# Kernel optimization log

Measured on AMD Instinct MI355X. Metric: run time of the kernel, lower is better.

Reference implementation:

```python
import jax, jax.numpy as jnp
import numpy as np

NT, NJ = 100000, 300000
FT = FJ = 32
H, OUT = 64, 16
E_TJ = E_JT = 1000000
E_JJ = 2000000
# NormalParamExtractor default: biased_softplus(1.0) -> softplus(x + inv_softplus(1.0))
SP_BIAS = float(np.log(np.expm1(1.0)))


def setup_inputs() -> dict:
    key = jax.random.key(0)
    ks = jax.random.split(key, 64)
    ki = iter(range(64))
    def nrm(shape, fan_in):
        return jax.random.normal(ks[next(ki)], shape, jnp.float32) / np.sqrt(fan_in)
    d = {}
    d['x_torso'] = jax.random.normal(ks[next(ki)], (NT, FT), jnp.float32)
    d['x_joint'] = jax.random.normal(ks[next(ki)], (NJ, FJ), jnp.float32)
    def edges(e, n_src, n_dst):
        src = jax.random.randint(ks[next(ki)], (e,), 0, n_src, jnp.int32)
        dst = jax.random.randint(ks[next(ki)], (e,), 0, n_dst, jnp.int32)
        return jnp.stack([src, dst])
    d['ei_tj'] = edges(E_TJ, NT, NJ)
    d['ei_jt'] = edges(E_JT, NJ, NT)
    d['ei_jj'] = edges(E_JJ, NJ, NJ)
    d['w0_t'] = nrm((FT, H), FT); d['b0_t'] = jnp.zeros((H,), jnp.float32)
    d['w0_j'] = nrm((FJ, H), FJ); d['b0_j'] = jnp.zeros((H,), jnp.float32)
    for layer in ('c1', 'c2'):
        for et in ('tj', 'jt', 'jj'):
            d[f'{layer}_{et}_rel_w'] = nrm((H, H), H)
            d[f'{layer}_{et}_rel_b'] = jnp.zeros((H,), jnp.float32)
            d[f'{layer}_{et}_root_w'] = nrm((H, H), H)
    d['w3_t'] = nrm((H, OUT), H); d['b3_t'] = jnp.zeros((OUT,), jnp.float32)
    d['w3_j'] = nrm((H, OUT), H); d['b3_j'] = jnp.zeros((OUT,), jnp.float32)
    return d


def _graph_conv(x_src, x_dst, ei, rel_w, rel_b, root_w, n_dst):
    # PyG GraphConv: lin_rel(sum_{j in N(i)} x_j) + lin_root(x_i)
    msg = jax.ops.segment_sum(x_src[ei[0]], ei[1], num_segments=n_dst)
    return msg @ rel_w + rel_b + x_dst @ root_w


def reference(x_torso, x_joint, ei_tj, ei_jt, ei_jj,
              w0_t, b0_t, w0_j, b0_j,
              c1_tj_rel_w, c1_tj_rel_b, c1_tj_root_w,
              c1_jt_rel_w, c1_jt_rel_b, c1_jt_root_w,
              c1_jj_rel_w, c1_jj_rel_b, c1_jj_root_w,
              c2_tj_rel_w, c2_tj_rel_b, c2_tj_root_w,
              c2_jt_rel_w, c2_jt_rel_b, c2_jt_root_w,
              c2_jj_rel_w, c2_jj_rel_b, c2_jj_root_w,
              w3_t, b3_t, w3_j, b3_j):
    # per-node-type input Linear
    h_t = x_torso @ w0_t + b0_t  # [NT, 64]
    h_j = x_joint @ w0_j + b0_j  # [NJ, 64]
    # hetero GraphConv layer 1 (to_hetero sums per-edge-type outputs on dst)
    t1 = _graph_conv(h_j, h_t, ei_jt, c1_jt_rel_w, c1_jt_rel_b, c1_jt_root_w, NT)
    j1 = (_graph_conv(h_t, h_j, ei_tj, c1_tj_rel_w, c1_tj_rel_b, c1_tj_root_w, NJ)
          + _graph_conv(h_j, h_j, ei_jj, c1_jj_rel_w, c1_jj_rel_b, c1_jj_root_w, NJ))
    h_t, h_j = jnp.tanh(t1), jnp.tanh(j1)
    # layer 2
    t2 = _graph_conv(h_j, h_t, ei_jt, c2_jt_rel_w, c2_jt_rel_b, c2_jt_root_w, NT)
    j2 = (_graph_conv(h_t, h_j, ei_tj, c2_tj_rel_w, c2_tj_rel_b, c2_tj_root_w, NJ)
          + _graph_conv(h_j, h_j, ei_jj, c2_jj_rel_w, c2_jj_rel_b, c2_jj_root_w, NJ))
    h_t, h_j = jnp.tanh(t2), jnp.tanh(j2)
    # output Linear + tanh per node type
    o_t = jnp.tanh(h_t @ w3_t + b3_t)  # [NT, 16]
    o_j = jnp.tanh(h_j @ w3_j + b3_j)  # [NJ, 16]
    # NormalParamExtractor: chunk last dim, biased softplus on scale
    loc_t, s_t = jnp.split(o_t, 2, axis=-1)
    loc_j, s_j = jnp.split(o_j, 2, axis=-1)
    scale_t = jax.nn.softplus(s_t + SP_BIAS)
    scale_j = jax.nn.softplus(s_j + SP_BIAS)
    return (loc_t, scale_t, loc_j, scale_j)
```

## Files before the change

### kernel.cpp

```cpp
#include <hip/hip_runtime.h>
#include <math.h>

constexpr int NT = 100000;
constexpr int NJ = 300000;
constexpr int E_TJ = 1000000, E_JT = 1000000, E_JJ = 2000000;
constexpr float SP_BIAS = 0.5413248546129181f;

__global__ void k_zero(int* __restrict__ p, int n) {
    int i = blockIdx.x * 256 + threadIdx.x;
    if (i < n) p[i] = 0;
}

__global__ void k_prep(const float* __restrict__ wa, const float* __restrict__ wb,
                       const float* __restrict__ ba, const float* __restrict__ bb,
                       float* __restrict__ wcomb, float* __restrict__ bcomb) {
    int i = blockIdx.x * 256 + threadIdx.x;
    if (i < 4096) wcomb[i] = wa[i] + wb[i];
    else if (i < 4160) bcomb[i - 4096] = ba[i - 4096] + bb[i - 4096];
}

__global__ void k_count(const int* __restrict__ dst, int E, int* __restrict__ deg) {
    int e = blockIdx.x * blockDim.x + threadIdx.x;
    if (e < E) atomicAdd(&deg[dst[e]], 1);
}

__global__ __launch_bounds__(1024) void k_bsum(const int* __restrict__ deg, int n,
                                               int* __restrict__ bsum) {
    __shared__ int s[1024];
    int i = blockIdx.x * 1024 + threadIdx.x;
    s[threadIdx.x] = (i < n) ? deg[i] : 0;
    __syncthreads();
    for (int d = 512; d > 0; d >>= 1) {
        if (threadIdx.x < d) s[threadIdx.x] += s[threadIdx.x + d];
        __syncthreads();
    }
    if (threadIdx.x == 0) bsum[blockIdx.x] = s[0];
}

__global__ __launch_bounds__(1024) void k_scan_bsum(int* bsum, int nb) {
    __shared__ int s[1024];
    int t = threadIdx.x;
    int v = (t < nb) ? bsum[t] : 0;
    s[t] = v;
    __syncthreads();
    for (int d = 1; d < 1024; d <<= 1) {
        int x = (t >= d) ? s[t - d] : 0;
        __syncthreads();
        s[t] += x;
        __syncthreads();
    }
    if (t < nb) bsum[t] = s[t] - v;
}

__global__ __launch_bounds__(1024) void k_scan_final(const int* __restrict__ deg, int n,
                                                     const int* __restrict__ bsum,
                                                     int* __restrict__ off,
                                                     int* __restrict__ cur) {
    __shared__ int s[1024];
    int t = threadIdx.x;
    int i = blockIdx.x * 1024 + t;
    int v = (i < n) ? deg[i] : 0;
    s[t] = v;
    __syncthreads();
    for (int d = 1; d < 1024; d <<= 1) {
        int x = (t >= d) ? s[t - d] : 0;
        __syncthreads();
        s[t] += x;
        __syncthreads();
    }
    int incl = s[t];
    int base = bsum[blockIdx.x];
    if (i < n) {
        int excl = base + incl - v;
        off[i] = excl;
        cur[i] = excl;
        if (i == n - 1) off[n] = base + incl;
    }
}

__global__ void k_fill(const int* __restrict__ src, const int* __restrict__ dst, int E,
                       int* __restrict__ cur, int* __restrict__ out_src, int src_ofs) {
    int e = blockIdx.x * blockDim.x + threadIdx.x;
    if (e < E) {
        int p = atomicAdd(&cur[dst[e]], 1);
        out_src[p] = (src[e] + src_ofs) * 64;
    }
}

__global__ __launch_bounds__(256) void k_in_linear(const float* __restrict__ x,
        const float* __restrict__ w, const float* __restrict__ b,
        float* __restrict__ h, int n) {
    __shared__ float ws_[32 * 64];
    __shared__ __align__(16) float xs_[512];
    for (int i = threadIdx.x; i < 32 * 64; i += 256) ws_[i] = w[i];
    __syncthreads();
    const int wslot = (threadIdx.x >> 6) & 3;
    const int lane = threadIdx.x & 63;
    const int lo = lane & 31;
    float* xsw = &xs_[wslot * 128];
    int wave = (blockIdx.x * 256 + threadIdx.x) >> 6;
    int nq = (n + 3) >> 2;
    int nwaves = gridDim.x * 4;
    float bv = b[lane];
    for (int q = wave; q < nq; q += nwaves) {
        int i0 = q * 4;
        int i1 = i0 + 1 < n ? i0 + 1 : n - 1;
        int i2 = i0 + 2 < n ? i0 + 2 : n - 1;
        int i3 = i0 + 3 < n ? i0 + 3 : n - 1;
        xsw[lane]      = (lane < 32) ? x[(size_t)i0 * 32 + lo] : x[(size_t)i1 * 32 + lo];
        xsw[64 + lane] = (lane < 32) ? x[(size_t)i2 * 32 + lo] : x[(size_t)i3 * 32 + lo];
        float r0 = bv, r1 = bv, r2 = bv, r3 = bv;
        const float4* xq = (const float4*)xsw;
        #pragma unroll
        for (int c = 0; c < 8; ++c) {
            float4 x0 = xq[c], x1 = xq[8 + c], x2 = xq[16 + c], x3 = xq[24 + c];
            float wA = ws_[(4 * c + 0) * 64 + lane];
            float wB = ws_[(4 * c + 1) * 64 + lane];
            float wC = ws_[(4 * c + 2) * 64 + lane];
            float wD = ws_[(4 * c + 3) * 64 + lane];
            r0 += x0.x * wA + x0.y * wB + x0.z * wC + x0.w * wD;
            r1 += x1.x * wA + x1.y * wB + x1.z * wC + x1.w * wD;
            r2 += x2.x * wA + x2.y * wB + x2.z * wC + x2.w * wD;
            r3 += x3.x * wA + x3.y * wB + x3.z * wC + x3.w * wD;
        }
        h[(size_t)i0 * 64 + lane] = r0;
        if (i0 + 1 < n) h[(size_t)i1 * 64 + lane] = r1;
        if (i0 + 2 < n) h[(size_t)i2 * 64 + lane] = r2;
        if (i0 + 3 < n) h[(size_t)i3 * 64 + lane] = r3;
    }
}

__global__ __launch_bounds__(256, 4) void k_transform(const float* __restrict__ h,
        const float* __restrict__ w, float* __restrict__ a, int n) {
    __shared__ float ws_[64 * 64];
    __shared__ __align__(16) float hs_[1024];
    for (int i = threadIdx.x; i < 64 * 64; i += 256) ws_[i] = w[i];
    __syncthreads();
    const int wslot = (threadIdx.x >> 6) & 3;
    const int lane = threadIdx.x & 63;
    float* hsw = &hs_[wslot * 256];
    int wave = (blockIdx.x * 256 + threadIdx.x) >> 6;
    int nq = (n + 3) >> 2;
    int nwaves = gridDim.x * 4;
    for (int q = wave; q < nq; q += nwaves) {
        int i0 = q * 4;
        int i1 = i0 + 1 < n ? i0 + 1 : n - 1;
        int i2 = i0 + 2 < n ? i0 + 2 : n - 1;
        int i3 = i0 + 3 < n ? i0 + 3 : n - 1;
        hsw[lane]       = h[(size_t)i0 * 64 + lane];
        hsw[64 + lane]  = h[(size_t)i1 * 64 + lane];
        hsw[128 + lane] = h[(size_t)i2 * 64 + lane];
        hsw[192 + lane] = h[(size_t)i3 * 64 + lane];
        float r0 = 0.f, r1 = 0.f, r2 = 0.f, r3 = 0.f;
        const float4* hq = (const float4*)hsw;
        #pragma unroll 4
        for (int c = 0; c < 16; ++c) {
            float4 h0 = hq[c], h1 = hq[16 + c], h2 = hq[32 + c], h3 = hq[48 + c];
            float wA = ws_[(4 * c + 0) * 64 + lane];
            float wB = ws_[(4 * c + 1) * 64 + lane];
            float wC = ws_[(4 * c + 2) * 64 + lane];
            float wD = ws_[(4 * c + 3) * 64 + lane];
            r0 += h0.x * wA + h0.y * wB + h0.z * wC + h0.w * wD;
            r1 += h1.x * wA + h1.y * wB + h1.z * wC + h1.w * wD;
            r2 += h2.x * wA + h2.y * wB + h2.z * wC + h2.w * wD;
            r3 += h3.x * wA + h3.y * wB + h3.z * wC + h3.w * wD;
        }
        a[(size_t)i0 * 64 + lane] = r0;
        if (i0 + 1 < n) a[(size_t)i1 * 64 + lane] = r1;
        if (i0 + 2 < n) a[(size_t)i2 * 64 + lane] = r2;
        if (i0 + 3 < n) a[(size_t)i3 * 64 + lane] = r3;
    }
}

__global__ __launch_bounds__(256, 4) void k_transform2(float* __restrict__ h,
        const float* __restrict__ wa, const float* __restrict__ wb,
        const float* __restrict__ bias, float* __restrict__ outa, int n) {
    __shared__ float wsa_[64 * 64];
    __shared__ float wsb_[64 * 64];
    __shared__ __align__(16) float hs_[1024];
    for (int i = threadIdx.x; i < 64 * 64; i += 256) { wsa_[i] = wa[i]; wsb_[i] = wb[i]; }
    __syncthreads();
    const int wslot = (threadIdx.x >> 6) & 3;
    const int lane = threadIdx.x & 63;
    float* hsw = &hs_[wslot * 256];
    int wave = (blockIdx.x * 256 + threadIdx.x) >> 6;
    int nq = (n + 3) >> 2;
    int nwaves = gridDim.x * 4;
    float bv = bias[lane];
    for (int q = wave; q < nq; q += nwaves) {
        int i0 = q * 4;
        int i1 = i0 + 1 < n ? i0 + 1 : n - 1;
        int i2 = i0 + 2 < n ? i0 + 2 : n - 1;
        int i3 = i0 + 3 < n ? i0 + 3 : n - 1;
        hsw[lane]       = h[(size_t)i0 * 64 + lane];
        hsw[64 + lane]  = h[(size_t)i1 * 64 + lane];
        hsw[128 + lane] = h[(size_t)i2 * 64 + lane];
        hsw[192 + lane] = h[(size_t)i3 * 64 + lane];
        float ra0 = 0.f, ra1 = 0.f, ra2 = 0.f, ra3 = 0.f;
        float rb0 = bv, rb1 = bv, rb2 = bv, rb3 = bv;
        const float4* hq = (const float4*)hsw;
        #pragma unroll 4
        for (int c = 0; c < 16; ++c) {
            float4 h0 = hq[c], h1 = hq[16 + c], h2 = hq[32 + c], h3 = hq[48 + c];
            float aA = wsa_[(4 * c + 0) * 64 + lane];
            float aB = wsa_[(4 * c + 1) * 64 + lane];
            float aC = wsa_[(4 * c + 2) * 64 + lane];
            float aD = wsa_[(4 * c + 3) * 64 + lane];
            ra0 += h0.x * aA + h0.y * aB + h0.z * aC + h0.w * aD;
            ra1 += h1.x * aA + h1.y * aB + h1.z * aC + h1.w * aD;
            ra2 += h2.x * aA + h2.y * aB + h2.z * aC + h2.w * aD;
            ra3 += h3.x * aA + h3.y * aB + h3.z * aC + h3.w * aD;
            float bA = wsb_[(4 * c + 0) * 64 + lane];
            float bB = wsb_[(4 * c + 1) * 64 + lane];
            float bC = wsb_[(4 * c + 2) * 64 + lane];
            float bD = wsb_[(4 * c + 3) * 64 + lane];
            rb0 += h0.x * bA + h0.y * bB + h0.z * bC + h0.w * bD;
            rb1 += h1.x * bA + h1.y * bB + h1.z * bC + h1.w * bD;
            rb2 += h2.x * bA + h2.y * bB + h2.z * bC + h2.w * bD;
            rb3 += h3.x * bA + h3.y * bB + h3.z * bC + h3.w * bD;
        }
        outa[(size_t)i0 * 64 + lane] = ra0;
        h[(size_t)i0 * 64 + lane] = rb0;
        if (i0 + 1 < n) { outa[(size_t)i1 * 64 + lane] = ra1; h[(size_t)i1 * 64 + lane] = rb1; }
        if (i0 + 2 < n) { outa[(size_t)i2 * 64 + lane] = ra2; h[(size_t)i2 * 64 + lane] = rb2; }
        if (i0 + 3 < n) { outa[(size_t)i3 * 64 + lane] = ra3; h[(size_t)i3 * 64 + lane] = rb3; }
    }
}

__global__ __launch_bounds__(256) void k_aggadd(const float* __restrict__ a,
        float* __restrict__ h,
        const int* __restrict__ off, const int* __restrict__ srcs, int n) {
    int wave = (blockIdx.x * 256 + threadIdx.x) >> 6;
    int lane = threadIdx.x & 63;
    int nwaves = gridDim.x * 4;
    for (int i = wave; i < n; i += nwaves) {
        int e0 = off[i], e1 = off[i + 1];
        float acc = h[(size_t)i * 64 + lane];
        for (int base = e0; base < e1; base += 64) {
            int rem = e1 - base;
            int cnt = rem < 64 ? rem : 64;
            int idx = (lane < cnt) ? srcs[base + lane] : 0;
            int k = 0;
            for (; k + 8 <= cnt; k += 8) {
                int s0 = __shfl(idx, k),     s1 = __shfl(idx, k + 1);
                int s2 = __shfl(idx, k + 2), s3 = __shfl(idx, k + 3);
                int s4 = __shfl(idx, k + 4), s5 = __shfl(idx, k + 5);
                int s6 = __shfl(idx, k + 6), s7 = __shfl(idx, k + 7);
                float v0 = a[(size_t)s0 + lane], v1 = a[(size_t)s1 + lane];
                float v2 = a[(size_t)s2 + lane], v3 = a[(size_t)s3 + lane];
                float v4 = a[(size_t)s4 + lane], v5 = a[(size_t)s5 + lane];
                float v6 = a[(size_t)s6 + lane], v7 = a[(size_t)s7 + lane];
                acc += ((v0 + v1) + (v2 + v3)) + ((v4 + v5) + (v6 + v7));
            }
            for (; k < cnt; ++k)
                acc += a[(size_t)__shfl(idx, k) + lane];
        }
        h[(size_t)i * 64 + lane] = tanhf(acc);
    }
}

__global__ __launch_bounds__(256) void k_out(const float* __restrict__ h,
        const float* __restrict__ w3, const float* __restrict__ b3,
        float* __restrict__ loc, float* __restrict__ scale, int n) {
    __shared__ float ws_[64 * 16];
    __shared__ __align__(16) float hs_[1024];
    for (int i = threadIdx.x; i < 64 * 16; i += 256) ws_[i] = w3[i];
    __syncthreads();
    const int wslot = (threadIdx.x >> 6) & 3;
    const int lane = threadIdx.x & 63;
    const int m = lane >> 4;
    const int o = lane & 15;
    float* hsw = &hs_[wslot * 256];
    int wave = (blockIdx.x * 256 + threadIdx.x) >> 6;
    int nq = (n + 3) >> 2;
    int nwaves = gridDim.x * 4;
    float bv = b3[o];
    for (int q = wave; q < nq; q += nwaves) {
        int i0 = q * 4;
        int i1 = i0 + 1 < n ? i0 + 1 : n - 1;
        int i2 = i0 + 2 < n ? i0 + 2 : n - 1;
        int i3 = i0 + 3 < n ? i0 + 3 : n - 1;
        hsw[lane]       = h[(size_t)i0 * 64 + lane];
        hsw[64 + lane]  = h[(size_t)i1 * 64 + lane];
        hsw[128 + lane] = h[(size_t)i2 * 64 + lane];
        hsw[192 + lane] = h[(size_t)i3 * 64 + lane];
        float acc = bv;
        const float4* hq = (const float4*)&hsw[m * 64];
        #pragma unroll
        for (int c = 0; c < 16; ++c) {
            float4 hv = hq[c];
            acc += hv.x * ws_[(4 * c + 0) * 16 + o];
            acc += hv.y * ws_[(4 * c + 1) * 16 + o];
            acc += hv.z * ws_[(4 * c + 2) * 16 + o];
            acc += hv.w * ws_[(4 * c + 3) * 16 + o];
        }
        int im = (m == 0) ? i0 : (m == 1) ? i1 : (m == 2) ? i2 : i3;
        bool valid = (i0 + m < n) || (m == 0);
        float v = tanhf(acc);
        if (valid) {
            if (o < 8) {
                loc[(size_t)im * 8 + o] = v;
            } else {
                float xx = v + SP_BIAS;
                float sp = (xx > 20.f) ? xx : log1pf(expf(xx));
                scale[(size_t)im * 8 + (o - 8)] = sp;
            }
        }
    }
}

extern "C" void kernel_launch(void* const* d_in, const int* in_sizes, int n_in,
                              void* d_out, int out_size, void* d_ws, size_t ws_size,
                              hipStream_t stream) {
    const float* x_t  = (const float*)d_in[0];
    const float* x_j  = (const float*)d_in[1];
    const int*   ei_tj = (const int*)d_in[2];
    const int*   ei_jt = (const int*)d_in[3];
    const int*   ei_jj = (const int*)d_in[4];
    const float* w0_t = (const float*)d_in[5];
    const float* b0_t = (const float*)d_in[6];
    const float* w0_j = (const float*)d_in[7];
    const float* b0_j = (const float*)d_in[8];
    const float* w3_t = (const float*)d_in[27];
    const float* b3_t = (const float*)d_in[28];
    const float* w3_j = (const float*)d_in[29];
    const float* b3_j = (const float*)d_in[30];

    float* fws   = (float*)d_ws;
    float* Q     = fws;
    float* P     = Q + (size_t)NT * 64;
    float* h_t   = P + (size_t)NJ * 64;
    float* h_j   = h_t + (size_t)NT * 64;
    float* wcomb = h_j + (size_t)NJ * 64;
    float* bcomb = wcomb + 64 * 64;
    int* iws    = (int*)(bcomb + 64);
    int* off_jt = iws;
    int* cur_jt = off_jt + NT + 1;
    int* off_cj = cur_jt + NT;
    int* cur_cj = off_cj + NJ + 1;
    int* src_jt = cur_cj + NJ;
    int* src_cj = src_jt + E_JT;
    int* bsum   = src_cj + E_TJ + E_JJ;

    size_t required = ((char*)(bsum + 1024)) - ((char*)d_ws);
    if (ws_size < required) return;

    int zcount = 2 * NT + 2 * NJ + 2;
    k_zero<<<(zcount + 255) / 256, 256, 0, stream>>>(iws, zcount);
    k_count<<<(E_JT + 255) / 256, 256, 0, stream>>>(ei_jt + E_JT, E_JT, cur_jt);
    k_count<<<(E_TJ + 255) / 256, 256, 0, stream>>>(ei_tj + E_TJ, E_TJ, cur_cj);
    k_count<<<(E_JJ + 255) / 256, 256, 0, stream>>>(ei_jj + E_JJ, E_JJ, cur_cj);

    auto scan = [&](int* cur, int* off, int n) {
        int nb = (n + 1023) / 1024;
        k_bsum<<<nb, 1024, 0, stream>>>(cur, n, bsum);
        k_scan_bsum<<<1, 1024, 0, stream>>>(bsum, nb);
        k_scan_final<<<nb, 1024, 0, stream>>>(cur, n, bsum, off, cur);
    };
    scan(cur_jt, off_jt, NT);
    scan(cur_cj, off_cj, NJ);

    k_fill<<<(E_JT + 255) / 256, 256, 0, stream>>>(ei_jt, ei_jt + E_JT, E_JT, cur_jt, src_jt, 0);
    k_fill<<<(E_TJ + 255) / 256, 256, 0, stream>>>(ei_tj, ei_tj + E_TJ, E_TJ, cur_cj, src_cj, 0);
    k_fill<<<(E_JJ + 255) / 256, 256, 0, stream>>>(ei_jj, ei_jj + E_JJ, E_JJ, cur_cj, src_cj, NT);

    k_in_linear<<<2048, 256, 0, stream>>>(x_t, w0_t, b0_t, h_t, NT);
    k_in_linear<<<2048, 256, 0, stream>>>(x_j, w0_j, b0_j, h_j, NJ);

    for (int l = 0; l < 2; ++l) {
        const float* tj_rel_w  = (const float*)d_in[9 + l * 9 + 0];
        const float* tj_rel_b  = (const float*)d_in[9 + l * 9 + 1];
        const float* tj_root_w = (const float*)d_in[9 + l * 9 + 2];
        const float* jt_rel_w  = (const float*)d_in[9 + l * 9 + 3];
        const float* jt_rel_b  = (const float*)d_in[9 + l * 9 + 4];
        const float* jt_root_w = (const float*)d_in[9 + l * 9 + 5];
        const float* jj_rel_w  = (const float*)d_in[9 + l * 9 + 6];
        const float* jj_rel_b  = (const float*)d_in[9 + l * 9 + 7];
        const float* jj_root_w = (const float*)d_in[9 + l * 9 + 8];

        k_prep<<<17, 256, 0, stream>>>(tj_root_w, jj_root_w, tj_rel_b, jj_rel_b, wcomb, bcomb);

        k_transform2<<<2048, 256, 0, stream>>>(h_t, tj_rel_w, jt_root_w, jt_rel_b, Q, NT);
        k_transform<<<2048, 256, 0, stream>>>(h_j, jt_rel_w, P, NJ);
        k_aggadd<<<2048, 256, 0, stream>>>(P, h_t, off_jt, src_jt, NT);
        k_transform2<<<2048, 256, 0, stream>>>(h_j, jj_rel_w, wcomb, bcomb, P, NJ);
        k_aggadd<<<2048, 256, 0, stream>>>(Q, h_j, off_cj, src_cj, NJ);
    }

    float* out = (float*)d_out;
    k_out<<<2048, 256, 0, stream>>>(h_t, w3_t, b3_t,
                                    out, out + (size_t)NT * 8, NT);
    k_out<<<2048, 256, 0, stream>>>(h_j, w3_j, b3_j,
                                    out + (size_t)2 * NT * 8,
                                    out + (size_t)2 * NT * 8 + (size_t)NJ * 8, NJ);
}
```

Baseline: 1.397 ms.

## Merge CSR count/fill launches and read transform rows directly via scalar addresses

The three per-edge-type count kernels and the three fill kernels are each merged into one launch. Each thread now handles four edges, and all of its atomics are issued together so more are in flight at once. The transform kernels no longer stage the four node rows through shared memory. Instead they compute wave-uniform row pointers with readfirstlane and load float4s straight from global memory, which drops the shared-memory round trip. The trade-off is broadcast global loads that rely on the cache, and the fill order within CSR segments changes, which could alter float summation order.

Result: slower. 1.469 ms (+5.1%).

```diff
diff --git a/kernel.cpp b/kernel.cpp
--- a/kernel.cpp
+++ b/kernel.cpp
@@ -19,9 +19,27 @@
     else if (i < 4160) bcomb[i - 4096] = ba[i - 4096] + bb[i - 4096];
 }
 
-__global__ void k_count(const int* __restrict__ dst, int E, int* __restrict__ deg) {
-    int e = blockIdx.x * blockDim.x + threadIdx.x;
-    if (e < E) atomicAdd(&deg[dst[e]], 1);
+__global__ void k_count3(const int* __restrict__ jt_e, const int* __restrict__ tj_e,
+                         const int* __restrict__ jj_e,
+                         int* __restrict__ cur_jt, int* __restrict__ cur_cj) {
+    constexpr int TOT = E_JT + E_TJ + E_JJ;
+    int t = blockIdx.x * blockDim.x + threadIdx.x;
+    int S = gridDim.x * blockDim.x;
+    int* ptr[4]; int dd[4]; bool ok[4];
+    #pragma unroll
+    for (int r = 0; r < 4; ++r) {
+        int g = t + r * S;
+        ok[r] = g < TOT;
+        int d = 0; int* cp = cur_jt;
+        if (ok[r]) {
+            if (g < E_JT)              { d = jt_e[E_JT + g]; cp = cur_jt; }
+            else if (g < E_JT + E_TJ)  { d = tj_e[E_TJ + (g - E_JT)]; cp = cur_cj; }
+            else                       { d = jj_e[E_JJ + (g - E_JT - E_TJ)]; cp = cur_cj; }
+        }
+        ptr[r] = cp; dd[r] = d;
+    }
+    #pragma unroll
+    for (int r = 0; r < 4; ++r) if (ok[r]) atomicAdd(&ptr[r][dd[r]], 1);
 }
 
 __global__ __launch_bounds__(1024) void k_bsum(const int* __restrict__ deg, int n,
@@ -78,13 +96,40 @@
     }
 }
 
-__global__ void k_fill(const int* __restrict__ src, const int* __restrict__ dst, int E,
-                       int* __restrict__ cur, int* __restrict__ out_src, int src_ofs) {
-    int e = blockIdx.x * blockDim.x + threadIdx.x;
-    if (e < E) {
-        int p = atomicAdd(&cur[dst[e]], 1);
-        out_src[p] = (src[e] + src_ofs) * 64;
-    }
+__global__ void k_fill3(const int* __restrict__ jt_e, const int* __restrict__ tj_e,
+                        const int* __restrict__ jj_e,
+                        int* __restrict__ cur_jt, int* __restrict__ cur_cj,
+                        int* __restrict__ src_jt, int* __restrict__ src_cj) {
+    constexpr int TOT = E_JT + E_TJ + E_JJ;
+    int t = blockIdx.x * blockDim.x + threadIdx.x;
+    int S = gridDim.x * blockDim.x;
+    int* curp[4]; int* outp[4]; int dd[4]; int sv[4]; bool ok[4];
+    #pragma unroll
+    for (int r = 0; r < 4; ++r) {
+        int g = t + r * S;
+        ok[r] = g < TOT;
+        int d = 0, s = 0; int* cp = cur_jt; int* op = src_jt;
+        if (ok[r]) {
+            if (g < E_JT) {
+                d = jt_e[E_JT + g]; s = jt_e[g] * 64;
+                cp = cur_jt; op = src_jt;
+            } else if (g < E_JT + E_TJ) {
+                int e = g - E_JT;
+                d = tj_e[E_TJ + e]; s = tj_e[e] * 64;
+                cp = cur_cj; op = src_cj;
+            } else {
+                int e = g - E_JT - E_TJ;
+                d = jj_e[E_JJ + e]; s = (jj_e[e] + NT) * 64;
+                cp = cur_cj; op = src_cj;
+            }
+        }
+        curp[r] = cp; outp[r] = op; dd[r] = d; sv[r] = s;
+    }
+    int pp[4];
+    #pragma unroll
+    for (int r = 0; r < 4; ++r) pp[r] = ok[r] ? atomicAdd(&curp[r][dd[r]], 1) : 0;
+    #pragma unroll
+    for (int r = 0; r < 4; ++r) if (ok[r]) outp[r][pp[r]] = sv[r];
 }
 
 __global__ __launch_bounds__(256) void k_in_linear(const float* __restrict__ x,
@@ -133,12 +178,9 @@
 __global__ __launch_bounds__(256, 4) void k_transform(const float* __restrict__ h,
         const float* __restrict__ w, float* __restrict__ a, int n) {
     __shared__ float ws_[64 * 64];
-    __shared__ __align__(16) float hs_[1024];
     for (int i = threadIdx.x; i < 64 * 64; i += 256) ws_[i] = w[i];
     __syncthreads();
-    const int wslot = (threadIdx.x >> 6) & 3;
     const int lane = threadIdx.x & 63;
-    float* hsw = &hs_[wslot * 256];
     int wave = (blockIdx.x * 256 + threadIdx.x) >> 6;
     int nq = (n + 3) >> 2;
     int nwaves = gridDim.x * 4;
@@ -147,15 +189,14 @@
         int i1 = i0 + 1 < n ? i0 + 1 : n - 1;
         int i2 = i0 + 2 < n ? i0 + 2 : n - 1;
         int i3 = i0 + 3 < n ? i0 + 3 : n - 1;
-        hsw[lane]       = h[(size_t)i0 * 64 + lane];
-        hsw[64 + lane]  = h[(size_t)i1 * 64 + lane];
-        hsw[128 + lane] = h[(size_t)i2 * 64 + lane];
-        hsw[192 + lane] = h[(size_t)i3 * 64 + lane];
+        const float4* h0p = (const float4*)(h + (size_t)__builtin_amdgcn_readfirstlane(i0) * 64);
+        const float4* h1p = (const float4*)(h + (size_t)__builtin_amdgcn_readfirstlane(i1) * 64);
+        const float4* h2p = (const float4*)(h + (size_t)__builtin_amdgcn_readfirstlane(i2) * 64);
+        const float4* h3p = (const float4*)(h + (size_t)__builtin_amdgcn_readfirstlane(i3) * 64);
         float r0 = 0.f, r1 = 0.f, r2 = 0.f, r3 = 0.f;
-        const float4* hq = (const float4*)hsw;
         #pragma unroll 4
         for (int c = 0; c < 16; ++c) {
-            float4 h0 = hq[c], h1 = hq[16 + c], h2 = hq[32 + c], h3 = hq[48 + c];
+            float4 h0 = h0p[c], h1 = h1p[c], h2 = h2p[c], h3 = h3p[c];
             float wA = ws_[(4 * c + 0) * 64 + lane];
             float wB = ws_[(4 * c + 1) * 64 + lane];
             float wC = ws_[(4 * c + 2) * 64 + lane];
@@ -177,12 +218,9 @@
         const float* __restrict__ bias, float* __restrict__ outa, int n) {
     __shared__ float wsa_[64 * 64];
     __shared__ float wsb_[64 * 64];
-    __shared__ __align__(16) float hs_[1024];
     for (int i = threadIdx.x; i < 64 * 64; i += 256) { wsa_[i] = wa[i]; wsb_[i] = wb[i]; }
     __syncthreads();
-    const int wslot = (threadIdx.x >> 6) & 3;
     const int lane = threadIdx.x & 63;
-    float* hsw = &hs_[wslot * 256];
     int wave = (blockIdx.x * 256 + threadIdx.x) >> 6;
     int nq = (n + 3) >> 2;
     int nwaves = gridDim.x * 4;
@@ -192,16 +230,15 @@
         int i1 = i0 + 1 < n ? i0 + 1 : n - 1;
         int i2 = i0 + 2 < n ? i0 + 2 : n - 1;
         int i3 = i0 + 3 < n ? i0 + 3 : n - 1;
-        hsw[lane]       = h[(size_t)i0 * 64 + lane];
-        hsw[64 + lane]  = h[(size_t)i1 * 64 + lane];
-        hsw[128 + lane] = h[(size_t)i2 * 64 + lane];
-        hsw[192 + lane] = h[(size_t)i3 * 64 + lane];
+        const float4* h0p = (const float4*)(h + (size_t)__builtin_amdgcn_readfirstlane(i0) * 64);
+        const float4* h1p = (const float4*)(h + (size_t)__builtin_amdgcn_readfirstlane(i1) * 64);
+        const float4* h2p = (const float4*)(h + (size_t)__builtin_amdgcn_readfirstlane(i2) * 64);
+        const float4* h3p = (const float4*)(h + (size_t)__builtin_amdgcn_readfirstlane(i3) * 64);
         float ra0 = 0.f, ra1 = 0.f, ra2 = 0.f, ra3 = 0.f;
         float rb0 = bv, rb1 = bv, rb2 = bv, rb3 = bv;
-        const float4* hq = (const float4*)hsw;
         #pragma unroll 4
         for (int c = 0; c < 16; ++c) {
-            float4 h0 = hq[c], h1 = hq[16 + c], h2 = hq[32 + c], h3 = hq[48 + c];
+            float4 h0 = h0p[c], h1 = h1p[c], h2 = h2p[c], h3 = h3p[c];
             float aA = wsa_[(4 * c + 0) * 64 + lane];
             float aB = wsa_[(4 * c + 1) * 64 + lane];
             float aC = wsa_[(4 * c + 2) * 64 + lane];
@@ -347,22 +384,24 @@
 
     int zcount = 2 * NT + 2 * NJ + 2;
     k_zero<<<(zcount + 255) / 256, 256, 0, stream>>>(iws, zcount);
-    k_count<<<(E_JT + 255) / 256, 256, 0, stream>>>(ei_jt + E_JT, E_JT, cur_jt);
-    k_count<<<(E_TJ + 255) / 256, 256, 0, stream>>>(ei_tj + E_TJ, E_TJ, cur_cj);
-    k_count<<<(E_JJ + 255) / 256, 256, 0, stream>>>(ei_jj + E_JJ, E_JJ, cur_cj);
-
-    auto scan = [&](int* cur, int* off, int n) {
-        int nb = (n + 1023) / 1024;
-        k_bsum<<<nb, 1024, 0, stream>>>(cur, n, bsum);
-        k_scan_bsum<<<1, 1024, 0, stream>>>(bsum, nb);
-        k_scan_final<<<nb, 1024, 0, stream>>>(cur, n, bsum, off, cur);
-    };
-    scan(cur_jt, off_jt, NT);
-    scan(cur_cj, off_cj, NJ);
-
-    k_fill<<<(E_JT + 255) / 256, 256, 0, stream>>>(ei_jt, ei_jt + E_JT, E_JT, cur_jt, src_jt, 0);
-    k_fill<<<(E_TJ + 255) / 256, 256, 0, stream>>>(ei_tj, ei_tj + E_TJ, E_TJ, cur_cj, src_cj, 0);
-    k_fill<<<(E_JJ + 255) / 256, 256, 0, stream>>>(ei_jj, ei_jj + E_JJ, E_JJ, cur_cj, src_cj, NT);
+    {
+        constexpr int TOT = E_JT + E_TJ + E_JJ;
+        int nth = (TOT + 3) / 4;
+        int nb = (nth + 255) / 256;
+        k_count3<<<nb, 256, 0, stream>>>(ei_jt, ei_tj, ei_jj, cur_jt, cur_cj);
+
+        auto scan = [&](int* cur, int* off, int n) {
+            int nbk = (n + 1023) / 1024;
+            k_bsum<<<nbk, 1024, 0, stream>>>(cur, n, bsum);
+            k_scan_bsum<<<1, 1024, 0, stream>>>(bsum, nbk);
+            k_scan_final<<<nbk, 1024, 0, stream>>>(cur, n, bsum, off, cur);
+        };
+        scan(cur_jt, off_jt, NT);
+        scan(cur_cj, off_cj, NJ);
+
+        k_fill3<<<nb, 256, 0, stream>>>(ei_jt, ei_tj, ei_jj,
+                                        cur_jt, cur_cj, src_jt, src_cj);
+    }
 
     k_in_linear<<<2048, 256, 0, stream>>>(x_t, w0_t, b0_t, h_t, NT);
     k_in_linear<<<2048, 256, 0, stream>>>(x_j, w0_j, b0_j, h_j, NJ);
```
